# Kernel tuning notes

Hardware: AMD Instinct MI355X
Metric: run time of the kernel (lower is better)

The kernel has to match this reference:

```python
import jax, jax.numpy as jnp
import numpy as np

STRIDE = 1
PAD = 1
POOL_K = 2
POOL_S = 2


def setup_inputs() -> dict:
    key = jax.random.key(0)
    k1, k2, k3 = jax.random.split(key, 3)
    N, Cin, H, W = 32, 64, 112, 112
    Cout, Kh, Kw = 128, 3, 3
    x = jax.random.normal(k1, (N, Cin, H, W), dtype=jnp.float32)
    # Kaiming-like scale for realism
    weight = jax.random.normal(k2, (Cout, Cin, Kh, Kw), dtype=jnp.float32) * (1.0 / np.sqrt(Cin * Kh * Kw))
    bias = jax.random.normal(k3, (Cout,), dtype=jnp.float32) * 0.01
    return {"x": x, "weight": weight, "bias": bias}


def reference(x, weight, bias):
    # Conv2d: NCHW input, OIHW weight, stride 1, pad 1 -> [N, Cout, 112, 112]
    y = jax.lax.conv_general_dilated(
        x, weight,
        window_strides=(STRIDE, STRIDE),
        padding=((PAD, PAD), (PAD, PAD)),
        dimension_numbers=("NCHW", "OIHW", "NCHW"),
    )
    y = jax.nn.relu(y + bias[None, :, None, None])
    # MaxPool2d 2x2 stride 2 -> [N, Cout, 56, 56]
    out = jax.lax.reduce_window(
        y,
        -jnp.inf,
        jax.lax.max,
        window_dimensions=(1, 1, POOL_K, POOL_K),
        window_strides=(1, 1, POOL_S, POOL_S),
        padding="VALID",
    )
    return out
```

## Files before the change

### kernel.cpp

```cpp
#include <hip/hip_runtime.h>

typedef __bf16 bf16x8 __attribute__((ext_vector_type(8)));
typedef float  f32x4  __attribute__((ext_vector_type(4)));

__device__ __forceinline__ unsigned short f2bf(float f) {
  unsigned u = __float_as_uint(f);
  u += 0x7FFFu + ((u >> 16) & 1u);
  return (unsigned short)(u >> 16);
}

#define WF_BYTES 147456

__global__ __launch_bounds__(64) void wxf_746(const float* __restrict__ w,
                                              unsigned short* __restrict__ wf) {
  const int b = blockIdx.x;
  const int lane = threadIdx.x;
  const int nb = b & 7, ck = (b >> 3) & 1, pos = b >> 4;
  const int kh = pos / 3, kw = pos % 3;
  const int co = nb * 16 + (lane & 15);
  const int ci0 = ck * 32 + ((lane >> 4) << 3);
  unsigned short* o = wf + ((size_t)(b * 64 + lane) << 3);
#pragma unroll
  for (int j = 0; j < 8; ++j)
    o[j] = f2bf(w[((co * 64 + ci0 + j) * 3 + kh) * 3 + kw]);
}

__global__ __launch_bounds__(256, 2) void conv_746(
    const float* __restrict__ x, const unsigned char* __restrict__ wsb,
    const float* __restrict__ bias, float* __restrict__ out) {
  __shared__ __align__(16) unsigned char lds[58368];
  const int bx = blockIdx.x;
  const int n = bx / 56, hpair = bx % 56, h0 = hpair * 2;
  const int tid = threadIdx.x;
  const int lane = tid & 63, wid = tid >> 6;
  const int wr = wid >> 1, wc2 = wid & 1;
  const int lw = lane & 15, hq = lane >> 4;

  float bb[4];
#pragma unroll
  for (int nf = 0; nf < 4; ++nf) bb[nf] = bias[wc2 * 64 + nf * 16 + lw];

  const f32x4 z4 = {0.f, 0.f, 0.f, 0.f};
  if (tid < 64) {
    const int r = tid >> 4, csel = (tid >> 3) & 1, s = tid & 7;
    const int col = csel ? 113 : 0;
    *(f32x4*)&lds[r * 14592 + col * 128 + s * 16] = z4;
  }
  const int wst = tid & 127;
  const int cig = tid >> 7;
  const float* xn = x + (size_t)n * 802816;
#pragma unroll
  for (int r = 0; r < 4; ++r) {
    const int h = h0 - 1 + r;
    if (h < 0 || h >= 112) {
      for (int off = tid * 16; off < 14592; off += 4096)
        *(f32x4*)&lds[r * 14592 + off] = z4;
    } else if (wst < 112) {
      const float* xr = xn + (size_t)h * 112 + wst;
      const int col = wst + 1;
      const int cbase = r * 14592 + col * 128;
      const int xorv = (col & 7) << 4;
#pragma unroll
      for (int i = 0; i < 16; ++i) {
        const int ci0 = cig * 32 + i * 2;
        const float f0 = xr[(size_t)ci0 * 12544];
        const float f1 = xr[(size_t)(ci0 + 1) * 12544];
        const unsigned pk = (unsigned)f2bf(f0) | ((unsigned)f2bf(f1) << 16);
        *(unsigned*)&lds[cbase + ((ci0 * 2) ^ xorv)] = pk;
      }
    }
  }
  __syncthreads();

  f32x4 acc[7][4];
#pragma unroll
  for (int f = 0; f < 7; ++f)
#pragma unroll
    for (int nf = 0; nf < 4; ++nf) acc[f][nf] = z4;

#pragma unroll
  for (int kh = 0; kh < 3; ++kh) {
#pragma unroll
    for (int kw = 0; kw < 3; ++kw) {
      const int xorv = ((lw + kw) & 7) << 4;
      const int abase0 = (wr + kh) * 14592 + (lw + kw) * 128;
#pragma unroll
      for (int ck = 0; ck < 2; ++ck) {
        bf16x8 bfr[4];
        const unsigned char* bp =
            wsb + (((size_t)(((kh * 3 + kw) * 2 + ck) * 8 + wc2 * 4) * 64 + lane) << 4);
#pragma unroll
        for (int nf = 0; nf < 4; ++nf)
          bfr[nf] = *(const bf16x8*)(bp + (nf << 10));
        const int abase = abase0 + ((ck * 64 + hq * 16) ^ xorv);
#pragma unroll
        for (int f = 0; f < 7; ++f) {
          const bf16x8 a = *(const bf16x8*)&lds[abase + f * 2048];
#pragma unroll
          for (int nf = 0; nf < 4; ++nf)
            acc[f][nf] = __builtin_amdgcn_mfma_f32_16x16x32_bf16(a, bfr[nf], acc[f][nf], 0, 0, 0);
        }
      }
    }
  }

  __syncthreads();
  float pl0[7][4], pl1[7][4];
#pragma unroll
  for (int f = 0; f < 7; ++f)
#pragma unroll
    for (int nf = 0; nf < 4; ++nf) {
      const float a0 = fmaxf(acc[f][nf][0] + bb[nf], 0.f);
      const float a1 = fmaxf(acc[f][nf][1] + bb[nf], 0.f);
      const float a2 = fmaxf(acc[f][nf][2] + bb[nf], 0.f);
      const float a3 = fmaxf(acc[f][nf][3] + bb[nf], 0.f);
      pl0[f][nf] = fmaxf(a0, a1);
      pl1[f][nf] = fmaxf(a2, a3);
    }
  float* pb = (float*)lds;
  if (wr == 0) {
#pragma unroll
    for (int f = 0; f < 7; ++f)
#pragma unroll
      for (int nf = 0; nf < 4; ++nf) {
        const int bse = wc2 * 3584 + (f * 8 + hq * 2) * 64 + nf * 16 + lw;
        pb[bse] = pl0[f][nf];
        pb[bse + 64] = pl1[f][nf];
      }
  }
  __syncthreads();
  float* pb2 = (float*)(lds + 28672);
  if (wr == 1) {
#pragma unroll
    for (int f = 0; f < 7; ++f)
#pragma unroll
      for (int nf = 0; nf < 4; ++nf) {
        const int bse = wc2 * 3584 + (f * 8 + hq * 2) * 64 + nf * 16 + lw;
        const float v0 = fmaxf(pl0[f][nf], pb[bse]);
        const float v1 = fmaxf(pl1[f][nf], pb[bse + 64]);
        const int ob = (wc2 * 64 + nf * 16 + lw) * 56 + f * 8 + hq * 2;
        pb2[ob] = v0;
        pb2[ob + 1] = v1;
      }
  }
  __syncthreads();
  const float* pb2c = (const float*)(lds + 28672);
#pragma unroll
  for (int i = 0; i < 7; ++i) {
    const int idx = i * 256 + tid;
    const int co = idx / 14, q = idx - co * 14;
    const f32x4 v = *(const f32x4*)&pb2c[co * 56 + q * 4];
    *(f32x4*)(out + (size_t)(n * 128 + co) * 3136 + hpair * 56 + q * 4) = v;
  }
}

__global__ __launch_bounds__(256) void naive_746(
    const float* __restrict__ x, const float* __restrict__ wt,
    const float* __restrict__ bias, float* __restrict__ out) {
  int idx = blockIdx.x * 256 + threadIdx.x;
  if (idx >= 12845056) return;
  int pw = idx % 56; int t = idx / 56;
  int ph = t % 56; t /= 56;
  int co = t % 128; int n = t / 128;
  float best = 0.f;
  for (int dh = 0; dh < 2; ++dh)
    for (int dw = 0; dw < 2; ++dw) {
      int oh = ph * 2 + dh, ow = pw * 2 + dw;
      float acc = bias[co];
      for (int ci = 0; ci < 64; ++ci) {
        const float* xp = x + ((size_t)(n * 64 + ci) * 112) * 112;
        const float* wp = wt + (co * 64 + ci) * 9;
        for (int kh = 0; kh < 3; ++kh) {
          int ih = oh + kh - 1; if (ih < 0 || ih >= 112) continue;
          for (int kw = 0; kw < 3; ++kw) {
            int iw = ow + kw - 1; if (iw < 0 || iw >= 112) continue;
            acc += xp[ih * 112 + iw] * wp[kh * 3 + kw];
          }
        }
      }
      best = fmaxf(best, fmaxf(acc, 0.f));
    }
  out[idx] = best;
}

extern "C" void kernel_launch(void* const* d_in, const int* in_sizes, int n_in,
                              void* d_out, int out_size, void* d_ws, size_t ws_size,
                              hipStream_t stream) {
  const float* x = (const float*)d_in[0];
  const float* w = (const float*)d_in[1];
  const float* b = (const float*)d_in[2];
  float* o = (float*)d_out;
  if (ws_size < (size_t)WF_BYTES) {
    naive_746<<<dim3((12845056 + 255) / 256), dim3(256), 0, stream>>>(x, w, b, o);
    return;
  }
  unsigned short* wf = (unsigned short*)d_ws;
  wxf_746<<<dim3(144), dim3(64), 0, stream>>>(w, wf);
  conv_746<<<dim3(1792), dim3(256), 0, stream>>>(x, (const unsigned char*)d_ws, b, o);
}
```

Before: 89.58 us.

## Double conv block to eight waves splitting output channels per wave

```diff
diff --git a/kernel.cpp b/kernel.cpp
--- a/kernel.cpp
+++ b/kernel.cpp
@@ -25,7 +25,7 @@
     o[j] = f2bf(w[((co * 64 + ci0 + j) * 3 + kh) * 3 + kw]);
 }
 
-__global__ __launch_bounds__(256, 2) void conv_746(
+__global__ __launch_bounds__(512, 4) void conv_746(
     const float* __restrict__ x, const unsigned char* __restrict__ wsb,
     const float* __restrict__ bias, float* __restrict__ out) {
   __shared__ __align__(16) unsigned char lds[58368];
@@ -33,12 +33,12 @@
   const int n = bx / 56, hpair = bx % 56, h0 = hpair * 2;
   const int tid = threadIdx.x;
   const int lane = tid & 63, wid = tid >> 6;
-  const int wr = wid >> 1, wc2 = wid & 1;
+  const int wr = wid >> 2, wc = wid & 3;
   const int lw = lane & 15, hq = lane >> 4;
 
-  float bb[4];
-#pragma unroll
-  for (int nf = 0; nf < 4; ++nf) bb[nf] = bias[wc2 * 64 + nf * 16 + lw];
+  float bb[2];
+#pragma unroll
+  for (int nf = 0; nf < 2; ++nf) bb[nf] = bias[(wc * 2 + nf) * 16 + lw];
 
   const f32x4 z4 = {0.f, 0.f, 0.f, 0.f};
   if (tid < 64) {
@@ -53,7 +53,7 @@
   for (int r = 0; r < 4; ++r) {
     const int h = h0 - 1 + r;
     if (h < 0 || h >= 112) {
-      for (int off = tid * 16; off < 14592; off += 4096)
+      for (int off = tid * 16; off < 14592; off += 8192)
         *(f32x4*)&lds[r * 14592 + off] = z4;
     } else if (wst < 112) {
       const float* xr = xn + (size_t)h * 112 + wst;
@@ -61,8 +61,8 @@
       const int cbase = r * 14592 + col * 128;
       const int xorv = (col & 7) << 4;
 #pragma unroll
-      for (int i = 0; i < 16; ++i) {
-        const int ci0 = cig * 32 + i * 2;
+      for (int i = 0; i < 8; ++i) {
+        const int ci0 = cig * 16 + i * 2;
         const float f0 = xr[(size_t)ci0 * 12544];
         const float f1 = xr[(size_t)(ci0 + 1) * 12544];
         const unsigned pk = (unsigned)f2bf(f0) | ((unsigned)f2bf(f1) << 16);
@@ -72,11 +72,11 @@
   }
   __syncthreads();
 
-  f32x4 acc[7][4];
+  f32x4 acc[7][2];
 #pragma unroll
   for (int f = 0; f < 7; ++f)
 #pragma unroll
-    for (int nf = 0; nf < 4; ++nf) acc[f][nf] = z4;
+    for (int nf = 0; nf < 2; ++nf) acc[f][nf] = z4;
 
 #pragma unroll
   for (int kh = 0; kh < 3; ++kh) {
@@ -86,30 +86,28 @@
       const int abase0 = (wr + kh) * 14592 + (lw + kw) * 128;
 #pragma unroll
       for (int ck = 0; ck < 2; ++ck) {
-        bf16x8 bfr[4];
+        bf16x8 bfr[2];
         const unsigned char* bp =
-            wsb + (((size_t)(((kh * 3 + kw) * 2 + ck) * 8 + wc2 * 4) * 64 + lane) << 4);
-#pragma unroll
-        for (int nf = 0; nf < 4; ++nf)
-          bfr[nf] = *(const bf16x8*)(bp + (nf << 10));
+            wsb + (((size_t)(((kh * 3 + kw) * 2 + ck) * 8 + wc * 2) * 64 + lane) << 4);
+        bfr[0] = *(const bf16x8*)bp;
+        bfr[1] = *(const bf16x8*)(bp + 1024);
         const int abase = abase0 + ((ck * 64 + hq * 16) ^ xorv);
 #pragma unroll
         for (int f = 0; f < 7; ++f) {
           const bf16x8 a = *(const bf16x8*)&lds[abase + f * 2048];
-#pragma unroll
-          for (int nf = 0; nf < 4; ++nf)
-            acc[f][nf] = __builtin_amdgcn_mfma_f32_16x16x32_bf16(a, bfr[nf], acc[f][nf], 0, 0, 0);
+          acc[f][0] = __builtin_amdgcn_mfma_f32_16x16x32_bf16(a, bfr[0], acc[f][0], 0, 0, 0);
+          acc[f][1] = __builtin_amdgcn_mfma_f32_16x16x32_bf16(a, bfr[1], acc[f][1], 0, 0, 0);
         }
       }
     }
   }
 
   __syncthreads();
-  float pl0[7][4], pl1[7][4];
+  float pl0[7][2], pl1[7][2];
 #pragma unroll
   for (int f = 0; f < 7; ++f)
 #pragma unroll
-    for (int nf = 0; nf < 4; ++nf) {
+    for (int nf = 0; nf < 2; ++nf) {
       const float a0 = fmaxf(acc[f][nf][0] + bb[nf], 0.f);
       const float a1 = fmaxf(acc[f][nf][1] + bb[nf], 0.f);
       const float a2 = fmaxf(acc[f][nf][2] + bb[nf], 0.f);
@@ -122,35 +120,37 @@
 #pragma unroll
     for (int f = 0; f < 7; ++f)
 #pragma unroll
-      for (int nf = 0; nf < 4; ++nf) {
-        const int bse = wc2 * 3584 + (f * 8 + hq * 2) * 64 + nf * 16 + lw;
-        pb[bse] = pl0[f][nf];
-        pb[bse + 64] = pl1[f][nf];
-      }
-  }
-  __syncthreads();
-  float* pb2 = (float*)(lds + 28672);
+      for (int nf = 0; nf < 2; ++nf) {
+        const int co = (wc * 2 + nf) * 16 + lw;
+        const int pw = f * 8 + hq * 2;
+        pb[co * 56 + pw] = pl0[f][nf];
+        pb[co * 56 + pw + 1] = pl1[f][nf];
+      }
+  }
+  __syncthreads();
   if (wr == 1) {
 #pragma unroll
     for (int f = 0; f < 7; ++f)
 #pragma unroll
-      for (int nf = 0; nf < 4; ++nf) {
-        const int bse = wc2 * 3584 + (f * 8 + hq * 2) * 64 + nf * 16 + lw;
-        const float v0 = fmaxf(pl0[f][nf], pb[bse]);
-        const float v1 = fmaxf(pl1[f][nf], pb[bse + 64]);
-        const int ob = (wc2 * 64 + nf * 16 + lw) * 56 + f * 8 + hq * 2;
-        pb2[ob] = v0;
-        pb2[ob + 1] = v1;
-      }
-  }
-  __syncthreads();
-  const float* pb2c = (const float*)(lds + 28672);
-#pragma unroll
-  for (int i = 0; i < 7; ++i) {
-    const int idx = i * 256 + tid;
-    const int co = idx / 14, q = idx - co * 14;
-    const f32x4 v = *(const f32x4*)&pb2c[co * 56 + q * 4];
-    *(f32x4*)(out + (size_t)(n * 128 + co) * 3136 + hpair * 56 + q * 4) = v;
+      for (int nf = 0; nf < 2; ++nf) {
+        const int co = (wc * 2 + nf) * 16 + lw;
+        const int pw = f * 8 + hq * 2;
+        const float v0 = fmaxf(pl0[f][nf], pb[co * 56 + pw]);
+        const float v1 = fmaxf(pl1[f][nf], pb[co * 56 + pw + 1]);
+        pb[co * 56 + pw] = v0;
+        pb[co * 56 + pw + 1] = v1;
+      }
+  }
+  __syncthreads();
+  const float* pbc = (const float*)lds;
+#pragma unroll
+  for (int i = 0; i < 4; ++i) {
+    const int idx = i * 512 + tid;
+    if (idx < 1792) {
+      const int co = idx / 14, q = idx - co * 14;
+      const f32x4 v = *(const f32x4*)&pbc[co * 56 + q * 4];
+      *(f32x4*)(out + (size_t)(n * 128 + co) * 3136 + hpair * 56 + q * 4) = v;
+    }
   }
 }
 
@@ -196,5 +196,5 @@
   }
   unsigned short* wf = (unsigned short*)d_ws;
   wxf_746<<<dim3(144), dim3(64), 0, stream>>>(w, wf);
-  conv_746<<<dim3(1792), dim3(256), 0, stream>>>(x, (const unsigned char*)d_ws, b, o);
-}
+  conv_746<<<dim3(1792), dim3(512), 0, stream>>>(x, (const unsigned char*)d_ws, b, o);
+}
```

Result: faster. 83.92 us (-6.3%).
